# Optimization experiments

Measured on AMD Instinct MI355X. Metric: run time of the kernel, lower is better.

## Reference

```python
import jax, jax.numpy as jnp
import numpy as np

N, F_IN, HID, H1, E = 50000, 512, 128, 4, 800000
NEG_SLOPE = 0.2

def setup_inputs() -> dict:
    key = jax.random.key(0)
    ks = jax.random.split(key, 10)
    s = lambda fan: 1.0 / np.sqrt(fan)
    x = jax.random.normal(ks[0], (N, F_IN), jnp.float32)
    edge_index = jax.random.randint(ks[1], (2, E), 0, N, jnp.int32)
    W1 = jax.random.normal(ks[2], (F_IN, H1 * HID), jnp.float32) * s(F_IN)
    a_src1 = jax.random.normal(ks[3], (H1, HID), jnp.float32) * s(HID)
    a_dst1 = jax.random.normal(ks[4], (H1, HID), jnp.float32) * s(HID)
    b1 = jnp.zeros((H1 * HID,), jnp.float32)
    W2 = jax.random.normal(ks[5], (H1 * HID, HID), jnp.float32) * s(H1 * HID)
    a_src2 = jax.random.normal(ks[6], (1, HID), jnp.float32) * s(HID)
    a_dst2 = jax.random.normal(ks[7], (1, HID), jnp.float32) * s(HID)
    b2 = jnp.zeros((HID,), jnp.float32)
    return {"x": x, "edge_index": edge_index, "W1": W1, "a_src1": a_src1,
            "a_dst1": a_dst1, "b1": b1, "W2": W2, "a_src2": a_src2,
            "a_dst2": a_dst2, "b2": b2}

def _gat(x, src, dst, W, a_src, a_dst, b, n):
    H, C = a_src.shape
    h = (x @ W).reshape(-1, H, C)                      # [N, H, C]
    # per-edge attention logits: alpha_src[src] + alpha_dst[dst]
    e = jax.nn.leaky_relu((h * a_src).sum(-1)[src] + (h * a_dst).sum(-1)[dst],
                          NEG_SLOPE)                   # [E', H]
    # segment softmax over destination node
    m = jax.ops.segment_max(e, dst, num_segments=n)
    p = jnp.exp(e - m[dst])
    denom = jax.ops.segment_sum(p, dst, num_segments=n)
    alpha = p / (denom[dst] + 1e-16)
    # weighted scatter-add aggregation
    out = jax.ops.segment_sum(h[src] * alpha[:, :, None], dst, num_segments=n)
    return out.reshape(-1, H * C) + b

def reference(x, edge_index, W1, a_src1, a_dst1, b1, W2, a_src2, a_dst2, b2):
    loops = jnp.arange(N, dtype=edge_index.dtype)      # add_self_loops=True
    src = jnp.concatenate([edge_index[0], loops])
    dst = jnp.concatenate([edge_index[1], loops])
    h = jax.nn.elu(_gat(x, src, dst, W1, a_src1, a_dst1, b1, N))
    return _gat(h, src, dst, W2, a_src2, a_dst2, b2, N)
```

## Files before the change

kernel.cpp:

```cpp
#include <hip/hip_runtime.h>
#include <hip/hip_bf16.h>
#include <math.h>

#define NEG_SLOPE 0.2f

constexpr int N_NODES = 50000;
constexpr int F_IN    = 512;
constexpr int HID     = 128;
constexpr int H1      = 4;
constexpr int E_EDGES = 800000;
constexpr int E_TOT   = E_EDGES + N_NODES;
constexpr int DEG_CAP = 64;

typedef __attribute__((ext_vector_type(8))) short short8;
typedef __attribute__((ext_vector_type(4))) float floatx4;
typedef __attribute__((ext_vector_type(4))) unsigned short ushort4v;

__device__ __forceinline__ unsigned short f2bf(float f) {
  union { float f; unsigned int u; } v; v.f = f;
  unsigned int u = v.u + 0x7FFFu + ((v.u >> 16) & 1u);
  return (unsigned short)(u >> 16);
}
__device__ __forceinline__ float bf_lo(unsigned int u) {
  union { unsigned int u; float f; } v; v.u = u << 16; return v.f;
}
__device__ __forceinline__ float bf_hi(unsigned int u) {
  union { unsigned int u; float f; } v; v.u = u & 0xFFFF0000u; return v.f;
}

__device__ __forceinline__ void store_val(float* p, float v) { *p = v; }
__device__ __forceinline__ void store_val(unsigned short* p, float v) { *p = f2bf(v); }

template <int CPT>
__device__ __forceinline__ void store_vec(unsigned short* p, const float* v) {
#pragma unroll
  for (int c = 0; c < CPT; c += 4) {
    ushort4v o;
#pragma unroll
    for (int j = 0; j < 4; ++j) o[j] = f2bf(v[c + j]);
    *(ushort4v*)(p + c) = o;
  }
}
template <int CPT>
__device__ __forceinline__ void store_vec(float* p, const float* v) {
#pragma unroll
  for (int c = 0; c < CPT; c += 4) *(float4*)(p + c) = *(const float4*)(v + c);
}

__device__ __forceinline__ void async_load16(const void* g, void* lds) {
  __builtin_amdgcn_global_load_lds(
      (const __attribute__((address_space(1))) unsigned int*)g,
      (__attribute__((address_space(3))) unsigned int*)lds, 16, 0, 0);
}

__global__ void prep_kernel(const float* __restrict__ W1, const float* __restrict__ W2,
                            unsigned short* __restrict__ W1t, unsigned short* __restrict__ W2t,
                            int* __restrict__ cnt) {
  int i = blockIdx.x * 256 + threadIdx.x;
  if (i < N_NODES) cnt[i] = 0;
  int j = i - N_NODES;
  if (j >= 0 && j < 512 * 512) {
    int n = j >> 9, k = j & 511;
    W1t[j] = f2bf(W1[k * 512 + n]);
  }
  int l = i - N_NODES - 512 * 512;
  if (l >= 0 && l < 128 * 512) {
    int n = l >> 9, k = l & 511;
    W2t[l] = f2bf(W2[k * 128 + n]);
  }
}

__global__ void fill_kernel(const int* __restrict__ ei, int* __restrict__ cnt,
                            int* __restrict__ adj) {
  int i = blockIdx.x * blockDim.x + threadIdx.x;
  if (i >= E_TOT) return;
  int s, d;
  if (i < E_EDGES) { s = ei[i]; d = ei[E_EDGES + i]; }
  else             { s = i - E_EDGES; d = s; }
  int pos = atomicAdd(&cnt[d], 1);
  if (pos < DEG_CAP) adj[d * DEG_CAP + pos] = s;
}

template <bool CVT_A, typename OT>
__global__ __launch_bounds__(256) void gemm_bf16_kernel(
    const void* __restrict__ Araw, const unsigned short* __restrict__ Bt,
    OT* __restrict__ C, const float* __restrict__ a_srcp, const float* __restrict__ a_dstp,
    float* __restrict__ alpha_src, float* __restrict__ alpha_dst,
    int M, int N, int K, int Hn, int nRowTiles) {
  __shared__ unsigned short As[128 * 32];
  __shared__ unsigned short Bs[128 * 32];
  __shared__ float red_s[128][2];
  __shared__ float red_d[128][2];

  int grp = blockIdx.x / (8 * Hn);
  int w8 = blockIdx.x % (8 * Hn);
  int head = w8 >> 3;
  int rowTile = grp * 8 + (w8 & 7);
  if (rowTile >= nRowTiles) return;
  int row0 = rowTile * 128;
  int col0 = head * 128;

  int tid = threadIdx.x;
  int lane = tid & 63, wave = tid >> 6;
  int wm = wave & 1, wn = wave >> 1;
  int l15 = lane & 15, quad = lane >> 4;

  floatx4 acc[4][4];
#pragma unroll
  for (int i = 0; i < 4; ++i)
#pragma unroll
    for (int j = 0; j < 4; ++j) acc[i][j] = (floatx4){0.f, 0.f, 0.f, 0.f};

  int seg_b = wave * 2;
  int r_in = (lane >> 2);
  int c8 = (lane & 3) * 8;

  for (int k0 = 0; k0 < K; k0 += 32) {
#pragma unroll
    for (int p = 0; p < 2; ++p) {
      int seg = seg_b + p;
      int r = seg * 16 + r_in;
      int gc = col0 + r;
      async_load16(Bt + (size_t)gc * K + k0 + c8, &Bs[seg * 512]);
    }
    if constexpr (CVT_A) {
      const float* Af = (const float*)Araw;
#pragma unroll
      for (int p = 0; p < 4; ++p) {
        int lin = tid + p * 256;
        int r = lin >> 3;
        int q = lin & 7;
        int gr = row0 + r; if (gr >= M) gr = M - 1;
        float4 f = *(const float4*)(Af + (size_t)gr * K + k0 + q * 4);
        ushort4v o;
        o[0] = f2bf(f.x); o[1] = f2bf(f.y); o[2] = f2bf(f.z); o[3] = f2bf(f.w);
        *(ushort4v*)&As[r * 32 + q * 4] = o;
      }
    } else {
      const unsigned short* Ab = (const unsigned short*)Araw;
#pragma unroll
      for (int p = 0; p < 2; ++p) {
        int seg = seg_b + p;
        int r = seg * 16 + r_in;
        int gr = row0 + r; if (gr >= M) gr = M - 1;
        async_load16(Ab + (size_t)gr * K + k0 + c8, &As[seg * 512]);
      }
    }
    __syncthreads();

    short8 a[4], b[4];
#pragma unroll
    for (int mi = 0; mi < 4; ++mi)
      a[mi] = *(const short8*)&As[(wm * 64 + mi * 16 + l15) * 32 + quad * 8];
#pragma unroll
    for (int ni = 0; ni < 4; ++ni)
      b[ni] = *(const short8*)&Bs[(wn * 64 + ni * 16 + l15) * 32 + quad * 8];
#pragma unroll
    for (int mi = 0; mi < 4; ++mi)
#pragma unroll
      for (int ni = 0; ni < 4; ++ni)
        acc[mi][ni] = __builtin_amdgcn_mfma_f32_16x16x32_bf16(a[mi], b[ni], acc[mi][ni], 0, 0, 0);
    __syncthreads();
  }

  float a_s[4], a_d[4];
#pragma unroll
  for (int ni = 0; ni < 4; ++ni) {
    int cih = wn * 64 + ni * 16 + l15;
    a_s[ni] = a_srcp[head * HID + cih];
    a_d[ni] = a_dstp[head * HID + cih];
  }

#pragma unroll
  for (int mi = 0; mi < 4; ++mi) {
#pragma unroll
    for (int r = 0; r < 4; ++r) {
      int rloc = wm * 64 + mi * 16 + quad * 4 + r;
      int grow = row0 + rloc;
      float ps = 0.f, pd = 0.f;
#pragma unroll
      for (int ni = 0; ni < 4; ++ni) {
        float v = acc[mi][ni][r];
        ps += v * a_s[ni];
        pd += v * a_d[ni];
        if (grow < M) {
          int gcol = col0 + wn * 64 + ni * 16 + l15;
          store_val(&C[(size_t)grow * N + gcol], v);
        }
      }
#pragma unroll
      for (int off = 1; off < 16; off <<= 1) {
        ps += __shfl_xor(ps, off);
        pd += __shfl_xor(pd, off);
      }
      if (l15 == 0) { red_s[rloc][wn] = ps; red_d[rloc][wn] = pd; }
    }
  }
  __syncthreads();
  if (tid < 128) {
    int grow = row0 + tid;
    if (grow < M) {
      alpha_src[(size_t)grow * Hn + head] = red_s[tid][0] + red_s[tid][1];
      alpha_dst[(size_t)grow * Hn + head] = red_d[tid][0] + red_d[tid][1];
    }
  }
}

template <int H, typename OT>
__global__ __launch_bounds__(64) void aggregate_kernel(
    const unsigned short* __restrict__ h, const float* __restrict__ asrc,
    const float* __restrict__ adst, const int* __restrict__ cnt,
    const int* __restrict__ adj, const float* __restrict__ bias,
    OT* __restrict__ out, int apply_elu) {
  constexpr int CPT = 8;
  constexpr int CH = H * HID;
  constexpr int NCH = CH / CPT;
  constexpr int SLOTS = 64 / NCH;
  __shared__ float p_sh[64 * H];
  __shared__ int ro_sh[64];
  int node = blockIdx.x;
  int lane = threadIdx.x;
  int deg = cnt[node];
  if (deg > DEG_CAP) deg = DEG_CAP;

  int s_i = 0;
  if (lane < deg) s_i = adj[node * DEG_CAP + lane];
  ro_sh[lane] = s_i * CH;

  float ar[H];
#pragma unroll
  for (int hh = 0; hh < H; ++hh) ar[hh] = (lane < deg) ? asrc[s_i * H + hh] : 0.f;
#pragma unroll
  for (int hh = 0; hh < H; ++hh) {
    float v = ar[hh] + adst[node * H + hh];
    v = (v > 0.f) ? v : NEG_SLOPE * v;
    float lg = (lane < deg) ? v : -1e30f;
#pragma unroll
    for (int o = 32; o; o >>= 1) lg = fmaxf(lg, __shfl_xor(lg, o));
    float p = (lane < deg) ? expf(v - lg) : 0.f;
    float s = p;
#pragma unroll
    for (int o = 32; o; o >>= 1) s += __shfl_xor(s, o);
    p_sh[lane * H + hh] = p * (1.f / (s + 1e-16f));
  }
  __syncthreads();

  int chlane = lane % NCH;
  int slot = lane / NCH;
  int ch = chlane * CPT;
  int head = ch >> 7;

  float acc[CPT];
#pragma unroll
  for (int c = 0; c < CPT; ++c) acc[c] = 0.f;

  auto body = [&](int e) {
    float w = p_sh[e * H + head];
    uint4 u = *(const uint4*)(h + (size_t)(unsigned)ro_sh[e] + ch);
    acc[0] += bf_lo(u.x) * w;  acc[1] += bf_hi(u.x) * w;
    acc[2] += bf_lo(u.y) * w;  acc[3] += bf_hi(u.y) * w;
    acc[4] += bf_lo(u.z) * w;  acc[5] += bf_hi(u.z) * w;
    acc[6] += bf_lo(u.w) * w;  acc[7] += bf_hi(u.w) * w;
  };
  int e = slot;
  for (; e + 7 * SLOTS < deg; e += 8 * SLOTS) {
    body(e); body(e + SLOTS); body(e + 2 * SLOTS); body(e + 3 * SLOTS);
    body(e + 4 * SLOTS); body(e + 5 * SLOTS); body(e + 6 * SLOTS); body(e + 7 * SLOTS);
  }
  for (; e + SLOTS < deg; e += 2 * SLOTS) { body(e); body(e + SLOTS); }
  for (; e < deg; e += SLOTS) body(e);

#pragma unroll
  for (int o = NCH; o < 64; o <<= 1)
#pragma unroll
    for (int c = 0; c < CPT; ++c) acc[c] += __shfl_xor(acc[c], o);

  if (slot == 0) {
    float r[CPT];
#pragma unroll
    for (int c = 0; c < CPT; ++c) {
      float t = acc[c] + bias[ch + c];
      if (apply_elu) t = (t > 0.f) ? t : (expf(t) - 1.f);
      r[c] = t;
    }
    store_vec<CPT>(&out[(size_t)node * CH + ch], r);
  }
}

extern "C" void kernel_launch(void* const* d_in, const int* in_sizes, int n_in,
                              void* d_out, int out_size, void* d_ws, size_t ws_size,
                              hipStream_t stream) {
  const float* x      = (const float*)d_in[0];
  const int*   ei     = (const int*)d_in[1];
  const float* W1     = (const float*)d_in[2];
  const float* a_src1 = (const float*)d_in[3];
  const float* a_dst1 = (const float*)d_in[4];
  const float* b1     = (const float*)d_in[5];
  const float* W2     = (const float*)d_in[6];
  const float* a_src2 = (const float*)d_in[7];
  const float* a_dst2 = (const float*)d_in[8];
  const float* b2     = (const float*)d_in[9];
  float* out = (float*)d_out;

  float* ws   = (float*)d_ws;
  float* as1  = ws;
  float* ad1  = as1 + N_NODES * H1;
  float* as2  = ad1 + N_NODES * H1;
  float* ad2  = as2 + N_NODES;
  unsigned short* bufA = (unsigned short*)(ad2 + N_NODES);
  unsigned short* bufB = bufA + (size_t)N_NODES * 512;
  unsigned short* hmidb = bufA;
  unsigned short* h1b   = bufB;
  unsigned short* h2b   = bufB;
  unsigned short* W1t   = bufB + (size_t)N_NODES * 512;
  unsigned short* W2t   = W1t + 512 * 512;
  int* cnt = (int*)(W2t + 128 * 512);
  int* adj = cnt + N_NODES;

  constexpr int NRT = (N_NODES + 127) / 128;
  constexpr int NRT8 = ((NRT + 7) / 8) * 8;
  constexpr int PREP_ITEMS = N_NODES + 512 * 512 + 128 * 512;

  prep_kernel<<<(PREP_ITEMS + 255) / 256, 256, 0, stream>>>(W1, W2, W1t, W2t, cnt);
  fill_kernel<<<(E_TOT + 255) / 256, 256, 0, stream>>>(ei, cnt, adj);

  gemm_bf16_kernel<true, unsigned short><<<NRT8 * H1, 256, 0, stream>>>(
      x, W1t, h1b, a_src1, a_dst1, as1, ad1, N_NODES, 512, 512, H1, NRT);
  aggregate_kernel<4, unsigned short><<<N_NODES, 64, 0, stream>>>(
      h1b, as1, ad1, cnt, adj, b1, hmidb, 1);

  gemm_bf16_kernel<false, unsigned short><<<NRT8, 256, 0, stream>>>(
      hmidb, W2t, h2b, a_src2, a_dst2, as2, ad2, N_NODES, 128, 512, 1, NRT);
  aggregate_kernel<1, float><<<N_NODES, 64, 0, stream>>>(
      h2b, as2, ad2, cnt, adj, b2, out, 0);
}
```

Measured before the change: 475.5 us.

## Pack four nodes per aggregate block and prefetch neighbor rows before softmax

```diff
diff --git a/kernel.cpp b/kernel.cpp
--- a/kernel.cpp
+++ b/kernel.cpp
@@ -14,6 +14,7 @@
 
 typedef __attribute__((ext_vector_type(8))) short short8;
 typedef __attribute__((ext_vector_type(4))) float floatx4;
+typedef __attribute__((ext_vector_type(2))) float f32x2;
 typedef __attribute__((ext_vector_type(4))) unsigned short ushort4v;
 
 __device__ __forceinline__ unsigned short f2bf(float f) {
@@ -207,29 +208,51 @@
 }
 
 template <int H, typename OT>
-__global__ __launch_bounds__(64) void aggregate_kernel(
+__global__ __launch_bounds__(256) void aggregate_kernel(
     const unsigned short* __restrict__ h, const float* __restrict__ asrc,
     const float* __restrict__ adst, const int* __restrict__ cnt,
     const int* __restrict__ adj, const float* __restrict__ bias,
-    OT* __restrict__ out, int apply_elu) {
+    OT* __restrict__ out, int apply_elu, int nNodes) {
   constexpr int CPT = 8;
   constexpr int CH = H * HID;
   constexpr int NCH = CH / CPT;
   constexpr int SLOTS = 64 / NCH;
-  __shared__ float p_sh[64 * H];
-  __shared__ int ro_sh[64];
-  int node = blockIdx.x;
-  int lane = threadIdx.x;
+  constexpr int NW = 4;
+  __shared__ float p_sh[NW][64 * H];
+  __shared__ int ro_sh[NW][64];
+
+  const int wv = threadIdx.x >> 6;
+  const int lane = threadIdx.x & 63;
+  const int node = blockIdx.x * NW + wv;
+  if (node >= nNodes) return;
   int deg = cnt[node];
   if (deg > DEG_CAP) deg = DEG_CAP;
 
   int s_i = 0;
   if (lane < deg) s_i = adj[node * DEG_CAP + lane];
-  ro_sh[lane] = s_i * CH;
-
   float ar[H];
 #pragma unroll
   for (int hh = 0; hh < H; ++hh) ar[hh] = (lane < deg) ? asrc[s_i * H + hh] : 0.f;
+  ro_sh[wv][lane] = s_i * (CH * 2);
+  asm volatile("s_waitcnt lgkmcnt(0)" ::: "memory");
+
+  const int chlane = lane % NCH;
+  const int slot = lane / NCH;
+  const int ch = chlane * CPT;
+  const int head = ch >> 7;
+  const char* hb = (const char*)h + ch * 2;
+
+  auto loadu = [&](uint4& U, int e) {
+    if (e < deg) U = *(const uint4*)(hb + (unsigned)ro_sh[wv][e]);
+    else         U = make_uint4(0u, 0u, 0u, 0u);
+  };
+
+  uint4 u0, u1, u2, u3, u4, u5, u6, u7;
+  loadu(u0, slot);             loadu(u1, slot + SLOTS);
+  loadu(u2, slot + 2 * SLOTS); loadu(u3, slot + 3 * SLOTS);
+  loadu(u4, slot + 4 * SLOTS); loadu(u5, slot + 5 * SLOTS);
+  loadu(u6, slot + 6 * SLOTS); loadu(u7, slot + 7 * SLOTS);
+
 #pragma unroll
   for (int hh = 0; hh < H; ++hh) {
     float v = ar[hh] + adst[node * H + hh];
@@ -237,50 +260,61 @@
     float lg = (lane < deg) ? v : -1e30f;
 #pragma unroll
     for (int o = 32; o; o >>= 1) lg = fmaxf(lg, __shfl_xor(lg, o));
-    float p = (lane < deg) ? expf(v - lg) : 0.f;
+    float p = (lane < deg) ? __expf(v - lg) : 0.f;
     float s = p;
 #pragma unroll
     for (int o = 32; o; o >>= 1) s += __shfl_xor(s, o);
-    p_sh[lane * H + hh] = p * (1.f / (s + 1e-16f));
-  }
-  __syncthreads();
-
-  int chlane = lane % NCH;
-  int slot = lane / NCH;
-  int ch = chlane * CPT;
-  int head = ch >> 7;
-
-  float acc[CPT];
-#pragma unroll
-  for (int c = 0; c < CPT; ++c) acc[c] = 0.f;
-
-  auto body = [&](int e) {
-    float w = p_sh[e * H + head];
-    uint4 u = *(const uint4*)(h + (size_t)(unsigned)ro_sh[e] + ch);
-    acc[0] += bf_lo(u.x) * w;  acc[1] += bf_hi(u.x) * w;
-    acc[2] += bf_lo(u.y) * w;  acc[3] += bf_hi(u.y) * w;
-    acc[4] += bf_lo(u.z) * w;  acc[5] += bf_hi(u.z) * w;
-    acc[6] += bf_lo(u.w) * w;  acc[7] += bf_hi(u.w) * w;
+    p_sh[wv][lane * H + hh] = p * (1.f / (s + 1e-16f));
+  }
+  asm volatile("s_waitcnt lgkmcnt(0)" ::: "memory");
+
+  f32x2 ac0 = {0.f, 0.f}, ac1 = {0.f, 0.f}, ac2v = {0.f, 0.f}, ac3 = {0.f, 0.f};
+  auto consume = [&](const uint4& U, int e) {
+    float w = p_sh[wv][(e & 63) * H + head];
+    f32x2 wp = {w, w};
+    f32x2 t;
+    t.x = bf_lo(U.x); t.y = bf_hi(U.x); ac0  += t * wp;
+    t.x = bf_lo(U.y); t.y = bf_hi(U.y); ac1  += t * wp;
+    t.x = bf_lo(U.z); t.y = bf_hi(U.z); ac2v += t * wp;
+    t.x = bf_lo(U.w); t.y = bf_hi(U.w); ac3  += t * wp;
   };
-  int e = slot;
-  for (; e + 7 * SLOTS < deg; e += 8 * SLOTS) {
-    body(e); body(e + SLOTS); body(e + 2 * SLOTS); body(e + 3 * SLOTS);
-    body(e + 4 * SLOTS); body(e + 5 * SLOTS); body(e + 6 * SLOTS); body(e + 7 * SLOTS);
-  }
-  for (; e + SLOTS < deg; e += 2 * SLOTS) { body(e); body(e + SLOTS); }
-  for (; e < deg; e += SLOTS) body(e);
-
-#pragma unroll
-  for (int o = NCH; o < 64; o <<= 1)
-#pragma unroll
-    for (int c = 0; c < CPT; ++c) acc[c] += __shfl_xor(acc[c], o);
+
+  int base = 0;
+  for (;;) {
+    int nb = base + 8 * SLOTS;
+    if (nb < deg) {
+      consume(u0, base + slot);             loadu(u0, nb + slot);
+      consume(u1, base + slot + SLOTS);     loadu(u1, nb + slot + SLOTS);
+      consume(u2, base + slot + 2 * SLOTS); loadu(u2, nb + slot + 2 * SLOTS);
+      consume(u3, base + slot + 3 * SLOTS); loadu(u3, nb + slot + 3 * SLOTS);
+      consume(u4, base + slot + 4 * SLOTS); loadu(u4, nb + slot + 4 * SLOTS);
+      consume(u5, base + slot + 5 * SLOTS); loadu(u5, nb + slot + 5 * SLOTS);
+      consume(u6, base + slot + 6 * SLOTS); loadu(u6, nb + slot + 6 * SLOTS);
+      consume(u7, base + slot + 7 * SLOTS); loadu(u7, nb + slot + 7 * SLOTS);
+      base = nb;
+    } else {
+      consume(u0, base + slot);             consume(u1, base + slot + SLOTS);
+      consume(u2, base + slot + 2 * SLOTS); consume(u3, base + slot + 3 * SLOTS);
+      consume(u4, base + slot + 4 * SLOTS); consume(u5, base + slot + 5 * SLOTS);
+      consume(u6, base + slot + 6 * SLOTS); consume(u7, base + slot + 7 * SLOTS);
+      break;
+    }
+  }
+
+#pragma unroll
+  for (int o = NCH; o < 64; o <<= 1) {
+    ac0.x  += __shfl_xor(ac0.x, o);  ac0.y  += __shfl_xor(ac0.y, o);
+    ac1.x  += __shfl_xor(ac1.x, o);  ac1.y  += __shfl_xor(ac1.y, o);
+    ac2v.x += __shfl_xor(ac2v.x, o); ac2v.y += __shfl_xor(ac2v.y, o);
+    ac3.x  += __shfl_xor(ac3.x, o);  ac3.y  += __shfl_xor(ac3.y, o);
+  }
 
   if (slot == 0) {
-    float r[CPT];
+    float r[CPT] = {ac0.x, ac0.y, ac1.x, ac1.y, ac2v.x, ac2v.y, ac3.x, ac3.y};
 #pragma unroll
     for (int c = 0; c < CPT; ++c) {
-      float t = acc[c] + bias[ch + c];
-      if (apply_elu) t = (t > 0.f) ? t : (expf(t) - 1.f);
+      float t = r[c] + bias[ch + c];
+      if (apply_elu) t = (t > 0.f) ? t : (__expf(t) - 1.f);
       r[c] = t;
     }
     store_vec<CPT>(&out[(size_t)node * CH + ch], r);
@@ -326,11 +360,11 @@
 
   gemm_bf16_kernel<true, unsigned short><<<NRT8 * H1, 256, 0, stream>>>(
       x, W1t, h1b, a_src1, a_dst1, as1, ad1, N_NODES, 512, 512, H1, NRT);
-  aggregate_kernel<4, unsigned short><<<N_NODES, 64, 0, stream>>>(
-      h1b, as1, ad1, cnt, adj, b1, hmidb, 1);
+  aggregate_kernel<4, unsigned short><<<(N_NODES + 3) / 4, 256, 0, stream>>>(
+      h1b, as1, ad1, cnt, adj, b1, hmidb, 1, N_NODES);
 
   gemm_bf16_kernel<false, unsigned short><<<NRT8, 256, 0, stream>>>(
       hmidb, W2t, h2b, a_src2, a_dst2, as2, ad2, N_NODES, 128, 512, 1, NRT);
-  aggregate_kernel<1, float><<<N_NODES, 64, 0, stream>>>(
-      h2b, as2, ad2, cnt, adj, b2, out, 0);
-}
+  aggregate_kernel<1, float><<<(N_NODES + 3) / 4, 256, 0, stream>>>(
+      h2b, as2, ad2, cnt, adj, b2, out, 0, N_NODES);
+}
```

Result: slower. 492.4 us (+3.5%).
